# Kernel optimization log

Hardware: AMD Instinct MI355X
Metric: run time of the kernel (lower is better)

Reference implementation:

```python
import jax, jax.numpy as jnp
import numpy as np

N, E, IN_FEATS, D, H, DIST_DIM, NBOUND = 10000, 160000, 128, 64, 4, 32, 31

def setup_inputs() -> dict:
    key = jax.random.key(0)
    ks = jax.random.split(key, 16)
    gain = 5.0 / 3.0  # tanh gain
    def xavier(k, shape):
        # xavier_normal over the last two dims (fan_in, fan_out) as torch does per-slice
        fan_in, fan_out = shape[-2], shape[-1]
        std = gain * np.sqrt(2.0 / (fan_in + fan_out))
        return jax.random.normal(k, shape, dtype=jnp.float32) * std
    inp = {
        'feat': jax.random.normal(ks[0], (N, IN_FEATS), dtype=jnp.float32),
        'locations': jax.random.normal(ks[1], (N, 3), dtype=jnp.float32),
        'src': jax.random.randint(ks[2], (E,), 0, N),
        'dst': jax.random.randint(ks[3], (E,), 0, N),
        'inter_ids': jax.random.randint(ks[4], (E, H), 0, N),
        'W_fc': xavier(ks[5], (IN_FEATS, H * D)),
        'embed_table': jax.random.normal(ks[6], (NBOUND + 1, DIST_DIM), dtype=jnp.float32),
        'G': xavier(ks[7], (H, DIST_DIM, D)),
        'attn_fc1': xavier(ks[8], (H, 2 * D, D)),
        'attn_fc2': xavier(ks[9], (H, 2 * D, D)),
        'attn_fc3': xavier(ks[10], (H, 2 * D, D)),
        'attn_fc': xavier(ks[11], (H, 3 * D, D)),
        'attn_out': xavier(ks[12], (H, D, 1)),
        'boundaries': jnp.linspace(0.1, 3.1, NBOUND).astype(jnp.float32),
    }
    return inp


def reference(feat, locations, W_fc, embed_table, G, attn_fc1, attn_fc2, attn_fc3,
              attn_fc, attn_out, boundaries, src, dst, inter_ids):
    n = feat.shape[0]
    h = (feat @ W_fc).reshape(n, H, D)                      # [N,H,D]
    pos = locations                                          # [N,3]
    src_pos = pos[src]                                       # [E,3]
    dst_pos = pos[dst]                                       # [E,3]
    inter_pos = pos[inter_ids]                               # [E,H,3]
    h_src = h[src]                                           # [E,H,D]
    h_dst = h[dst]                                           # [E,H,D]
    head_idx = jnp.arange(H)[None, :]
    inter_h = h[inter_ids, head_idx, :]                      # [E,H,D] per-head gather

    e_count = src.shape[0]
    dist1 = jnp.broadcast_to(jnp.linalg.norm(dst_pos - src_pos, axis=-1)[:, None], (e_count, H))
    dist2 = jnp.linalg.norm(dst_pos[:, None, :] - inter_pos, axis=-1)   # [E,H]
    dist_ = jnp.linalg.norm(src_pos[:, None, :] - inter_pos, axis=-1)   # [E,H]

    def dist_embed(dist):
        idx = jnp.searchsorted(boundaries, dist, side='left')  # torch.bucketize(right=False)
        e = embed_table[idx]                                   # [E,H,DIST_DIM]
        return jnp.einsum('ehk,hkd->ehd', e, G)                # [E,H,D]

    de1 = dist_embed(dist1)
    de2 = dist_embed(dist2)
    de_ = dist_embed(dist_)

    d1 = jnp.einsum('ehk,hkd->ehd', jnp.concatenate([h_src, de1], axis=-1), attn_fc1)
    d2 = jnp.einsum('ehk,hkd->ehd', jnp.concatenate([inter_h, de2], axis=-1), attn_fc2)
    d3 = jnp.einsum('ehk,hkd->ehd', jnp.concatenate([h_dst, de_], axis=-1), attn_fc3)

    h_c = jnp.tanh(jnp.einsum('ehk,hkd->ehd', jnp.concatenate([d1, d2, d3], axis=-1), attn_fc))
    e_score = jnp.einsum('ehd,hdo->eho', h_c, attn_out)[..., 0]        # [E,H]

    # edge softmax grouped by destination node
    m = jax.ops.segment_max(e_score, dst, num_segments=n)              # [N,H]
    ex = jnp.exp(e_score - m[dst])
    den = jax.ops.segment_sum(ex, dst, num_segments=n)                 # [N,H]
    a = ex / den[dst]                                                  # [E,H]

    ft = jax.ops.segment_sum(a[:, :, None] * h_src, dst, num_segments=n)  # [N,H,D]
    rst = jnp.mean(ft, axis=1)                                          # merge='mean' -> [N,D]
    return rst
```

## Files before the change

### kernel.cpp

```cpp
#include <hip/hip_runtime.h>
#include <hip/hip_fp16.h>
#include <math.h>

#define N_NODES 10000
#define E_EDGES 160000
#define DMODEL 64
#define H 4
#define NBOUND 31
#define SLOTS 64
#define QREC 1024

typedef _Float16 half8 __attribute__((ext_vector_type(8)));
typedef float floatx4 __attribute__((ext_vector_type(4)));

__device__ __forceinline__ void mm4(const float* __restrict__ S, int aoff,
                                    int astride, int boff, int i0, int j,
                                    int Kdim, float o[4]) {
  float a0 = 0.f, a1 = 0.f, a2 = 0.f, a3 = 0.f;
  for (int t4 = 0; t4 < (Kdim >> 2); ++t4) {
    float4 f0 = *(const float4*)&S[aoff + (i0 + 0) * astride + t4 * 4];
    float4 f1 = *(const float4*)&S[aoff + (i0 + 1) * astride + t4 * 4];
    float4 f2 = *(const float4*)&S[aoff + (i0 + 2) * astride + t4 * 4];
    float4 f3 = *(const float4*)&S[aoff + (i0 + 3) * astride + t4 * 4];
    float b0 = S[boff + (t4 * 4 + 0) * 64 + j];
    float b1 = S[boff + (t4 * 4 + 1) * 64 + j];
    float b2 = S[boff + (t4 * 4 + 2) * 64 + j];
    float b3 = S[boff + (t4 * 4 + 3) * 64 + j];
    a0 += f0.x * b0 + f0.y * b1 + f0.z * b2 + f0.w * b3;
    a1 += f1.x * b0 + f1.y * b1 + f1.z * b2 + f1.w * b3;
    a2 += f2.x * b0 + f2.y * b1 + f2.z * b2 + f2.w * b3;
    a3 += f3.x * b0 + f3.y * b1 + f3.z * b2 + f3.w * b3;
  }
  o[0] = a0; o[1] = a1; o[2] = a2; o[3] = a3;
}

__device__ __forceinline__ int didx(const float* __restrict__ bnd2, float d) {
  int g = (int)(d * 10.0f);
  g = (g < 0) ? 0 : ((g > 31) ? 31 : g);
  g += (bnd2[g + 1] < d) ? 1 : 0;
  g -= (bnd2[g] >= d) ? 1 : 0;
  return g;
}

__global__ __launch_bounds__(512) void prep_kernel(
    const float* __restrict__ fc1, const float* __restrict__ fc2,
    const float* __restrict__ fc3, const float* __restrict__ fcc,
    const float* __restrict__ Wfc, const float* __restrict__ G,
    const float* __restrict__ emb, const float* __restrict__ pos,
    __half* __restrict__ bigWT, __half* __restrict__ U16,
    int* __restrict__ cnt, float4* __restrict__ pos4) {
  __shared__ __align__(16) float S[12288];
  int bi = blockIdx.x;
  int tid = threadIdx.x;
  if (bi >= 36) {
    int n = (bi - 36) * 512 + tid;
    if (n < N_NODES) {
      cnt[n] = 0;
      pos4[n] = make_float4(pos[n * 3], pos[n * 3 + 1], pos[n * 3 + 2], 0.f);
    }
    return;
  }
  int ca = bi / 12;
  int kh = bi % 12;
  int k = kh >> 2, h = kh & 3;
  const float* fck = (k == 0) ? fc1 : (k == 1) ? fc2 : fc3;
  fck += h * 128 * 64;
  const float* F = fcc + h * 192 * 64 + k * 64 * 64;
  int j = tid & 63, ig = tid >> 6;
  float o[4];
  if (ca < 2) {
    #pragma unroll
    for (int u = 0; u < 2; ++u) {
      ((float4*)S)[u * 512 + tid] = ((const float4*)F)[u * 512 + tid];
      ((float4*)(S + 4096))[u * 512 + tid] = ((const float4*)fck)[u * 512 + tid];
    }
    __syncthreads();
    #pragma unroll
    for (int rg = 0; rg < 2; ++rg) {
      int i0 = ig * 8 + rg * 4;
      mm4(S, 4096, 64, 0, i0, j, 64, o);
      S[8192 + (i0 + 0) * 64 + j] = o[0];
      S[8192 + (i0 + 1) * 64 + j] = o[1];
      S[8192 + (i0 + 2) * 64 + j] = o[2];
      S[8192 + (i0 + 3) * 64 + j] = o[3];
    }
    __syncthreads();
    int rbase = (ca == 0) ? 0 : 64;
    #pragma unroll
    for (int u = 0; u < 2; ++u) {
      int fi = u * 512 + tid;
      int i = fi >> 4, c4 = fi & 15;
      ((float4*)(S + 4096))[fi] =
          ((const float4*)(Wfc + (rbase + i) * 256 + h * 64))[c4];
    }
    __syncthreads();
    if (k == 0) {
      #pragma unroll
      for (int u = 0; u < 8; ++u) {
        int idx = u * 512 + tid;
        int i = idx >> 6, jj = idx & 63;
        bigWT[(h * 64 + jj) * 128 + rbase + i] = __float2half(S[4096 + idx]);
      }
    }
    #pragma unroll
    for (int rg = 0; rg < 2; ++rg) {
      int i0 = ig * 8 + rg * 4;
      mm4(S, 4096, 64, 8192, i0, j, 64, o);
      int rb = ((k + 1) * 256 + h * 64 + j) * 128 + rbase;
      bigWT[rb + i0 + 0] = __float2half(o[0]);
      bigWT[rb + i0 + 1] = __float2half(o[1]);
      bigWT[rb + i0 + 2] = __float2half(o[2]);
      bigWT[rb + i0 + 3] = __float2half(o[3]);
    }
    return;
  }
  #pragma unroll
  for (int u = 0; u < 2; ++u) {
    ((float4*)S)[u * 512 + tid] = ((const float4*)F)[u * 512 + tid];
    ((float4*)(S + 4096))[u * 512 + tid] =
        ((const float4*)(fck + 4096))[u * 512 + tid];
  }
  __syncthreads();
  #pragma unroll
  for (int rg = 0; rg < 2; ++rg) {
    int i0 = ig * 8 + rg * 4;
    mm4(S, 4096, 64, 0, i0, j, 64, o);
    S[8192 + (i0 + 0) * 64 + j] = o[0];
    S[8192 + (i0 + 1) * 64 + j] = o[1];
    S[8192 + (i0 + 2) * 64 + j] = o[2];
    S[8192 + (i0 + 3) * 64 + j] = o[3];
  }
  __syncthreads();
  ((float4*)S)[tid] = ((const float4*)(G + h * 2048))[tid];
  if (tid < 256) ((float4*)(S + 2048))[tid] = ((const float4*)emb)[tid];
  __syncthreads();
  {
    int i0 = ig * 4;
    mm4(S, 0, 64, 8192, i0, j, 64, o);
    S[3072 + (i0 + 0) * 64 + j] = o[0];
    S[3072 + (i0 + 1) * 64 + j] = o[1];
    S[3072 + (i0 + 2) * 64 + j] = o[2];
    S[3072 + (i0 + 3) * 64 + j] = o[3];
  }
  __syncthreads();
  {
    int i0 = ig * 4;
    mm4(S, 2048, 32, 3072, i0, j, 32, o);
    int base = k * 8192 + h * 2048;
    U16[base + (i0 + 0) * 64 + j] = __float2half(o[0]);
    U16[base + (i0 + 1) * 64 + j] = __float2half(o[1]);
    U16[base + (i0 + 2) * 64 + j] = __float2half(o[2]);
    U16[base + (i0 + 3) * 64 + j] = __float2half(o[3]);
  }
}

__global__ __launch_bounds__(256) void edge_kernel(
    const float4* __restrict__ pos4, const int* __restrict__ src,
    const int* __restrict__ dst, const int* __restrict__ inter,
    const float* __restrict__ boundaries, int* __restrict__ cnt,
    uint4* __restrict__ ebuf) {
  __shared__ float Sb[48];
  int tid = threadIdx.x;
  if (tid < NBOUND) Sb[tid + 1] = boundaries[tid];
  if (tid == NBOUND) { Sb[0] = -INFINITY; Sb[32] = INFINITY; }
  int e = blockIdx.x * 256 + tid;
  int s = src[e], t = dst[e];
  int p = atomicAdd(&cnt[t], 1);
  int4 iv = *(const int4*)&inter[e * 4];
  int itarr[4] = {iv.x, iv.y, iv.z, iv.w};
  float4 sp = pos4[s];
  float4 tp = pos4[t];
  float4 ip0 = pos4[itarr[0]];
  float4 ip1 = pos4[itarr[1]];
  float4 ip2 = pos4[itarr[2]];
  float4 ip3 = pos4[itarr[3]];
  __syncthreads();
  float dx = tp.x - sp.x, dy = tp.y - sp.y, dz = tp.z - sp.z;
  float dist1 = sqrtf(dx * dx + dy * dy + dz * dz);
  unsigned i1 = (unsigned)didx(Sb, dist1);
  float4 ips[4] = {ip0, ip1, ip2, ip3};
  unsigned w3 = 0, q20 = 0, q_0 = 0;
  #pragma unroll
  for (int hh = 0; hh < 4; ++hh) {
    float4 ip = ips[hh];
    float ax = tp.x - ip.x, ay = tp.y - ip.y, az = tp.z - ip.z;
    float dist2 = sqrtf(ax * ax + ay * ay + az * az);
    float bx = sp.x - ip.x, by = sp.y - ip.y, bz = sp.z - ip.z;
    float dist_ = sqrtf(bx * bx + by * by + bz * bz);
    unsigned idx2 = (unsigned)didx(Sb, dist2);
    unsigned idx_ = (unsigned)didx(Sb, dist_);
    if (hh == 0) { q20 = idx2; q_0 = idx_; }
    else w3 |= (idx2 | (idx_ << 5)) << ((hh - 1) * 10);
  }
  uint4 rec;
  rec.x = (unsigned)s | ((unsigned)itarr[0] << 16);
  rec.y = (unsigned)itarr[1] | ((unsigned)itarr[2] << 16);
  rec.z = (unsigned)itarr[3] | (i1 << 16) | (q20 << 21) | (q_0 << 26);
  rec.w = w3;
  if (p < SLOTS) ebuf[t * SLOTS + p] = rec;
}

#define EROW 264

__global__ __launch_bounds__(256) void gemm_kernel(
    const float* __restrict__ feat, const __half* __restrict__ bigWT,
    __half* __restrict__ qall) {
  __shared__ __align__(16) __half Esm[4][16][EROW];
  int bi = blockIdx.x;
  int tid = threadIdx.x;
  int bx = bi % 157, by = bi / 157;
  int wv = tid >> 6, l = tid & 63;
  int m0 = bx * 64 + wv * 16;
  int n0 = by * 256;
  int lm = l & 15, lk = (l >> 4) * 8;
  int arow = m0 + lm;
  if (arow >= N_NODES) arow = N_NODES - 1;
  const float* fp = feat + arow * 128 + lk;
  const _Float16* bp = (const _Float16*)bigWT + lk;
  half8 a[4];
  #pragma unroll
  for (int kt = 0; kt < 4; ++kt) {
    float4 u0 = *(const float4*)(fp + kt * 32);
    float4 u1 = *(const float4*)(fp + kt * 32 + 4);
    half8 t;
    t[0] = (_Float16)u0.x; t[1] = (_Float16)u0.y;
    t[2] = (_Float16)u0.z; t[3] = (_Float16)u0.w;
    t[4] = (_Float16)u1.x; t[5] = (_Float16)u1.y;
    t[6] = (_Float16)u1.z; t[7] = (_Float16)u1.w;
    a[kt] = t;
  }
  #pragma unroll
  for (int nt = 0; nt < 16; ++nt) {
    floatx4 acc = (floatx4){0.f, 0.f, 0.f, 0.f};
    #pragma unroll
    for (int kt = 0; kt < 4; ++kt) {
      half8 b = *(const half8*)(bp + (n0 + nt * 16 + lm) * 128 + kt * 32);
      acc = __builtin_amdgcn_mfma_f32_16x16x32_f16(a[kt], b, acc, 0, 0, 0);
    }
    int dd = nt * 16 + lm;
    #pragma unroll
    for (int r4 = 0; r4 < 4; ++r4)
      Esm[wv][(l >> 4) * 4 + r4][dd] = __float2half(acc[r4]);
  }
  __syncthreads();
  int row = l >> 2;
  int j0 = (l & 3) * 64;
  int m = m0 + row;
  if (m < N_NODES) {
    #pragma unroll
    for (int u = 0; u < 8; ++u) {
      uint4 v = *(const uint4*)&Esm[wv][row][j0 + u * 8];
      *(uint4*)&qall[m * QREC + by * 256 + j0 + u * 8] = v;
    }
  }
}

__device__ __forceinline__ float dpp_bfly_sum16(float v) {
  int x;
  x = __builtin_amdgcn_update_dpp(0, __float_as_int(v), 0xB1, 0xf, 0xf, true);
  v += __int_as_float(x);
  x = __builtin_amdgcn_update_dpp(0, __float_as_int(v), 0x4E, 0xf, 0xf, true);
  v += __int_as_float(x);
  x = __builtin_amdgcn_update_dpp(0, __float_as_int(v), 0x141, 0xf, 0xf, true);
  v += __int_as_float(x);
  x = __builtin_amdgcn_update_dpp(0, __float_as_int(v), 0x140, 0xf, 0xf, true);
  v += __int_as_float(x);
  return v;
}

union H4u { uint2 u; __half2 h[2]; };

__device__ __forceinline__ float tanh_dot(H4u A, H4u B, H4u C, H4u X, H4u Y,
                                          H4u Z, float4 a4) {
  __half2 z0 = __hadd2(__hadd2(A.h[0], B.h[0]), __hadd2(C.h[0], X.h[0]));
  z0 = __hadd2(z0, __hadd2(Y.h[0], Z.h[0]));
  __half2 z1 = __hadd2(__hadd2(A.h[1], B.h[1]), __hadd2(C.h[1], X.h[1]));
  z1 = __hadd2(z1, __hadd2(Y.h[1], Z.h[1]));
  float2 f0 = __half22float2(z0);
  float2 f1 = __half22float2(z1);
  const float K = 2.885390082f;
  float p0 = __builtin_amdgcn_exp2f(f0.x * K);
  float p1 = __builtin_amdgcn_exp2f(f0.y * K);
  float p2 = __builtin_amdgcn_exp2f(f1.x * K);
  float p3 = __builtin_amdgcn_exp2f(f1.y * K);
  float r0 = __builtin_amdgcn_rcpf(p0 + 1.0f);
  float r1 = __builtin_amdgcn_rcpf(p1 + 1.0f);
  float r2 = __builtin_amdgcn_rcpf(p2 + 1.0f);
  float r3 = __builtin_amdgcn_rcpf(p3 + 1.0f);
  float dot = a4.x * r0;
  dot = fmaf(a4.y, r1, dot);
  dot = fmaf(a4.z, r2, dot);
  dot = fmaf(a4.w, r3, dot);
  float asum = (a4.x + a4.y) + (a4.z + a4.w);
  return fmaf(-2.0f, dot, asum);
}

__device__ __forceinline__ float4 h4_to_f4(uint2 u) {
  union { uint2 ui; __half2 h[2]; } cc;
  cc.ui = u;
  float2 a = __half22float2(cc.h[0]);
  float2 b = __half22float2(cc.h[1]);
  return make_float4(a.x, a.y, b.x, b.y);
}

__device__ __forceinline__ void dec_rec(uint4 r, int h, int* s, int* it,
                                        unsigned* i1, unsigned* q2,
                                        unsigned* q_) {
  *s = (int)(r.x & 0xffff);
  *it = (h == 0) ? (int)(r.x >> 16)
      : (h == 1) ? (int)(r.y & 0xffff)
      : (h == 2) ? (int)(r.y >> 16) : (int)(r.z & 0xffff);
  *i1 = (r.z >> 16) & 31;
  if (h == 0) {
    *q2 = (r.z >> 21) & 31;
    *q_ = (r.z >> 26) & 31;
  } else {
    unsigned f = r.w >> ((h - 1) * 10);
    *q2 = f & 31;
    *q_ = (f >> 5) & 31;
  }
}

__global__ __launch_bounds__(256) void score_agg_kernel(
    const int* __restrict__ cnt, const uint4* __restrict__ ebuf,
    const __half* __restrict__ qall, const __half* __restrict__ U16,
    const float* __restrict__ aout, float* __restrict__ out) {
  __shared__ uint4 recs[SLOTS];
  __shared__ float4 sm_num[4][64];
  __shared__ float sm_den[4][4];
  int tid = threadIdx.x;
  int w = tid >> 6, lane = tid & 63;
  int h = lane >> 4, c = lane & 15;
  int n = blockIdx.x;
  int deg = cnt[n];
  if (deg > SLOTS) deg = SLOTS;
  if (tid < deg) recs[tid] = ebuf[n * SLOTS + tid];
  H4u C;
  C.u = *(const uint2*)(qall + n * QREC + 768 + h * 64 + c * 4);
  const float4 a4 = *((const float4*)(aout + h * 64) + c);
  __syncthreads();
  float4 num = make_float4(0.f, 0.f, 0.f, 0.f);
  float den = 0.f;
  int hc4 = h * 64 + c * 4;
  for (int i = w; i < deg; i += 8) {
    int iB = i + 4;
    int vB = (iB < deg);
    uint4 rA = recs[i];
    uint4 rB = recs[vB ? iB : i];
    int sA, itA, sB, itB;
    unsigned i1A, q2A, q_A, i1B, q2B, q_B;
    dec_rec(rA, h, &sA, &itA, &i1A, &q2A, &q_A);
    dec_rec(rB, h, &sB, &itB, &i1B, &q2B, &q_B);
    H4u A0, B0, X0, Y0, Z0, A1, B1, X1, Y1, Z1;
    uint2 hr0, hr1;
    hr0 = *(const uint2*)(qall + sA * QREC + hc4);
    A0.u = *(const uint2*)(qall + sA * QREC + 256 + hc4);
    B0.u = *(const uint2*)(qall + itA * QREC + 512 + hc4);
    X0.u = *(const uint2*)(U16 + (h * 32 + (int)i1A) * 64 + c * 4);
    Y0.u = *(const uint2*)(U16 + 8192 + (h * 32 + (int)q2A) * 64 + c * 4);
    Z0.u = *(const uint2*)(U16 + 16384 + (h * 32 + (int)q_A) * 64 + c * 4);
    hr1 = *(const uint2*)(qall + sB * QREC + hc4);
    A1.u = *(const uint2*)(qall + sB * QREC + 256 + hc4);
    B1.u = *(const uint2*)(qall + itB * QREC + 512 + hc4);
    X1.u = *(const uint2*)(U16 + (h * 32 + (int)i1B) * 64 + c * 4);
    Y1.u = *(const uint2*)(U16 + 8192 + (h * 32 + (int)q2B) * 64 + c * 4);
    Z1.u = *(const uint2*)(U16 + 16384 + (h * 32 + (int)q_B) * 64 + c * 4);
    float v0 = tanh_dot(A0, B0, C, X0, Y0, Z0, a4);
    float v1 = tanh_dot(A1, B1, C, X1, Y1, Z1, a4);
    v0 = dpp_bfly_sum16(v0);
    v1 = dpp_bfly_sum16(v1);
    float ex0 = __expf(v0);
    float ex1 = vB ? __expf(v1) : 0.f;
    float4 hv0 = h4_to_f4(hr0);
    float4 hv1 = h4_to_f4(hr1);
    num.x += ex0 * hv0.x + ex1 * hv1.x;
    num.y += ex0 * hv0.y + ex1 * hv1.y;
    num.z += ex0 * hv0.z + ex1 * hv1.z;
    num.w += ex0 * hv0.w + ex1 * hv1.w;
    den += ex0 + ex1;
  }
  sm_num[w][lane] = num;
  if (c == 0) sm_den[w][h] = den;
  __syncthreads();
  if (tid < 64) {
    float4 n0 = sm_num[0][lane], n1 = sm_num[1][lane];
    float4 n2 = sm_num[2][lane], n3 = sm_num[3][lane];
    float dt = sm_den[0][h] + sm_den[1][h] + sm_den[2][h] + sm_den[3][h];
    float4 t = make_float4(0.f, 0.f, 0.f, 0.f);
    if (deg > 0) {
      float inv = 1.0f / dt;
      t.x = (n0.x + n1.x + n2.x + n3.x) * inv;
      t.y = (n0.y + n1.y + n2.y + n3.y) * inv;
      t.z = (n0.z + n1.z + n2.z + n3.z) * inv;
      t.w = (n0.w + n1.w + n2.w + n3.w) * inv;
    }
    t.x += __shfl_xor(t.x, 16); t.y += __shfl_xor(t.y, 16);
    t.z += __shfl_xor(t.z, 16); t.w += __shfl_xor(t.w, 16);
    t.x += __shfl_xor(t.x, 32); t.y += __shfl_xor(t.y, 32);
    t.z += __shfl_xor(t.z, 32); t.w += __shfl_xor(t.w, 32);
    if (h == 0) {
      t.x *= 0.25f; t.y *= 0.25f; t.z *= 0.25f; t.w *= 0.25f;
      *(float4*)&out[n * 64 + c * 4] = t;
    }
  }
}

extern "C" void kernel_launch(void* const* d_in, const int* in_sizes, int n_in,
                              void* d_out, int out_size, void* d_ws,
                              size_t ws_size, hipStream_t stream) {
  const float* feat = (const float*)d_in[0];
  const float* loc = (const float*)d_in[1];
  const int* src = (const int*)d_in[2];
  const int* dst = (const int*)d_in[3];
  const int* inter = (const int*)d_in[4];
  const float* Wfc = (const float*)d_in[5];
  const float* emb = (const float*)d_in[6];
  const float* G = (const float*)d_in[7];
  const float* fc1 = (const float*)d_in[8];
  const float* fc2 = (const float*)d_in[9];
  const float* fc3 = (const float*)d_in[10];
  const float* fcc = (const float*)d_in[11];
  const float* aout = (const float*)d_in[12];
  const float* bnd = (const float*)d_in[13];
  float* out = (float*)d_out;

  __half* qall = (__half*)d_ws;
  __half* bigWT = qall + N_NODES * QREC;
  __half* U16 = bigWT + 1024 * 128;
  uint4* ebuf = (uint4*)(U16 + 3 * H * 2048);
  int* cnt = (int*)(ebuf + N_NODES * SLOTS);
  float4* pos4 = (float4*)(cnt + N_NODES);

  prep_kernel<<<56, 512, 0, stream>>>(fc1, fc2, fc3, fcc, Wfc, G, emb, loc,
                                      bigWT, U16, cnt, pos4);
  edge_kernel<<<E_EDGES / 256, 256, 0, stream>>>(pos4, src, dst, inter, bnd,
                                                 cnt, ebuf);
  gemm_kernel<<<628, 256, 0, stream>>>(feat, bigWT, qall);
  score_agg_kernel<<<N_NODES, 256, 0, stream>>>(cnt, ebuf, qall, U16, aout,
                                                out);
}
```

Before: 182.2 us.

## Fuse edge preprocessing, U16 precompute and node GEMM into one launch

The edge binning kernel, the distance-embedding table precompute and the node GEMM now run as block ranges of a single fused kernel launch. The prep kernel keeps only the bigWT weight folding and the node init. This removes one kernel launch and the serialization between the edge and GEMM stages, letting their blocks overlap. The cost is a shared-memory union sized for the GEMM path and heterogeneous blocks whose durations differ.

```diff
diff --git a/kernel.cpp b/kernel.cpp
--- a/kernel.cpp
+++ b/kernel.cpp
@@ -45,15 +45,14 @@
 __global__ __launch_bounds__(512) void prep_kernel(
     const float* __restrict__ fc1, const float* __restrict__ fc2,
     const float* __restrict__ fc3, const float* __restrict__ fcc,
-    const float* __restrict__ Wfc, const float* __restrict__ G,
-    const float* __restrict__ emb, const float* __restrict__ pos,
-    __half* __restrict__ bigWT, __half* __restrict__ U16,
-    int* __restrict__ cnt, float4* __restrict__ pos4) {
+    const float* __restrict__ Wfc, const float* __restrict__ pos,
+    __half* __restrict__ bigWT, int* __restrict__ cnt,
+    float4* __restrict__ pos4) {
   __shared__ __align__(16) float S[12288];
   int bi = blockIdx.x;
   int tid = threadIdx.x;
-  if (bi >= 36) {
-    int n = (bi - 36) * 512 + tid;
+  if (bi >= 24) {
+    int n = (bi - 24) * 512 + tid;
     if (n < N_NODES) {
       cnt[n] = 0;
       pos4[n] = make_float4(pos[n * 3], pos[n * 3 + 1], pos[n * 3 + 2], 0.f);
@@ -68,57 +67,10 @@
   const float* F = fcc + h * 192 * 64 + k * 64 * 64;
   int j = tid & 63, ig = tid >> 6;
   float o[4];
-  if (ca < 2) {
-    #pragma unroll
-    for (int u = 0; u < 2; ++u) {
-      ((float4*)S)[u * 512 + tid] = ((const float4*)F)[u * 512 + tid];
-      ((float4*)(S + 4096))[u * 512 + tid] = ((const float4*)fck)[u * 512 + tid];
-    }
-    __syncthreads();
-    #pragma unroll
-    for (int rg = 0; rg < 2; ++rg) {
-      int i0 = ig * 8 + rg * 4;
-      mm4(S, 4096, 64, 0, i0, j, 64, o);
-      S[8192 + (i0 + 0) * 64 + j] = o[0];
-      S[8192 + (i0 + 1) * 64 + j] = o[1];
-      S[8192 + (i0 + 2) * 64 + j] = o[2];
-      S[8192 + (i0 + 3) * 64 + j] = o[3];
-    }
-    __syncthreads();
-    int rbase = (ca == 0) ? 0 : 64;
-    #pragma unroll
-    for (int u = 0; u < 2; ++u) {
-      int fi = u * 512 + tid;
-      int i = fi >> 4, c4 = fi & 15;
-      ((float4*)(S + 4096))[fi] =
-          ((const float4*)(Wfc + (rbase + i) * 256 + h * 64))[c4];
-    }
-    __syncthreads();
-    if (k == 0) {
-      #pragma unroll
-      for (int u = 0; u < 8; ++u) {
-        int idx = u * 512 + tid;
-        int i = idx >> 6, jj = idx & 63;
-        bigWT[(h * 64 + jj) * 128 + rbase + i] = __float2half(S[4096 + idx]);
-      }
-    }
-    #pragma unroll
-    for (int rg = 0; rg < 2; ++rg) {
-      int i0 = ig * 8 + rg * 4;
-      mm4(S, 4096, 64, 8192, i0, j, 64, o);
-      int rb = ((k + 1) * 256 + h * 64 + j) * 128 + rbase;
-      bigWT[rb + i0 + 0] = __float2half(o[0]);
-      bigWT[rb + i0 + 1] = __float2half(o[1]);
-      bigWT[rb + i0 + 2] = __float2half(o[2]);
-      bigWT[rb + i0 + 3] = __float2half(o[3]);
-    }
-    return;
-  }
   #pragma unroll
   for (int u = 0; u < 2; ++u) {
     ((float4*)S)[u * 512 + tid] = ((const float4*)F)[u * 512 + tid];
-    ((float4*)(S + 4096))[u * 512 + tid] =
-        ((const float4*)(fck + 4096))[u * 512 + tid];
+    ((float4*)(S + 4096))[u * 512 + tid] = ((const float4*)fck)[u * 512 + tid];
   }
   __syncthreads();
   #pragma unroll
@@ -131,84 +83,156 @@
     S[8192 + (i0 + 3) * 64 + j] = o[3];
   }
   __syncthreads();
-  ((float4*)S)[tid] = ((const float4*)(G + h * 2048))[tid];
-  if (tid < 256) ((float4*)(S + 2048))[tid] = ((const float4*)emb)[tid];
-  __syncthreads();
-  {
-    int i0 = ig * 4;
-    mm4(S, 0, 64, 8192, i0, j, 64, o);
-    S[3072 + (i0 + 0) * 64 + j] = o[0];
-    S[3072 + (i0 + 1) * 64 + j] = o[1];
-    S[3072 + (i0 + 2) * 64 + j] = o[2];
-    S[3072 + (i0 + 3) * 64 + j] = o[3];
-  }
-  __syncthreads();
-  {
-    int i0 = ig * 4;
-    mm4(S, 2048, 32, 3072, i0, j, 32, o);
-    int base = k * 8192 + h * 2048;
-    U16[base + (i0 + 0) * 64 + j] = __float2half(o[0]);
-    U16[base + (i0 + 1) * 64 + j] = __float2half(o[1]);
-    U16[base + (i0 + 2) * 64 + j] = __float2half(o[2]);
-    U16[base + (i0 + 3) * 64 + j] = __float2half(o[3]);
-  }
-}
-
-__global__ __launch_bounds__(256) void edge_kernel(
-    const float4* __restrict__ pos4, const int* __restrict__ src,
-    const int* __restrict__ dst, const int* __restrict__ inter,
-    const float* __restrict__ boundaries, int* __restrict__ cnt,
-    uint4* __restrict__ ebuf) {
-  __shared__ float Sb[48];
-  int tid = threadIdx.x;
-  if (tid < NBOUND) Sb[tid + 1] = boundaries[tid];
-  if (tid == NBOUND) { Sb[0] = -INFINITY; Sb[32] = INFINITY; }
-  int e = blockIdx.x * 256 + tid;
-  int s = src[e], t = dst[e];
-  int p = atomicAdd(&cnt[t], 1);
-  int4 iv = *(const int4*)&inter[e * 4];
-  int itarr[4] = {iv.x, iv.y, iv.z, iv.w};
-  float4 sp = pos4[s];
-  float4 tp = pos4[t];
-  float4 ip0 = pos4[itarr[0]];
-  float4 ip1 = pos4[itarr[1]];
-  float4 ip2 = pos4[itarr[2]];
-  float4 ip3 = pos4[itarr[3]];
-  __syncthreads();
-  float dx = tp.x - sp.x, dy = tp.y - sp.y, dz = tp.z - sp.z;
-  float dist1 = sqrtf(dx * dx + dy * dy + dz * dz);
-  unsigned i1 = (unsigned)didx(Sb, dist1);
-  float4 ips[4] = {ip0, ip1, ip2, ip3};
-  unsigned w3 = 0, q20 = 0, q_0 = 0;
-  #pragma unroll
-  for (int hh = 0; hh < 4; ++hh) {
-    float4 ip = ips[hh];
-    float ax = tp.x - ip.x, ay = tp.y - ip.y, az = tp.z - ip.z;
-    float dist2 = sqrtf(ax * ax + ay * ay + az * az);
-    float bx = sp.x - ip.x, by = sp.y - ip.y, bz = sp.z - ip.z;
-    float dist_ = sqrtf(bx * bx + by * by + bz * bz);
-    unsigned idx2 = (unsigned)didx(Sb, dist2);
-    unsigned idx_ = (unsigned)didx(Sb, dist_);
-    if (hh == 0) { q20 = idx2; q_0 = idx_; }
-    else w3 |= (idx2 | (idx_ << 5)) << ((hh - 1) * 10);
-  }
-  uint4 rec;
-  rec.x = (unsigned)s | ((unsigned)itarr[0] << 16);
-  rec.y = (unsigned)itarr[1] | ((unsigned)itarr[2] << 16);
-  rec.z = (unsigned)itarr[3] | (i1 << 16) | (q20 << 21) | (q_0 << 26);
-  rec.w = w3;
-  if (p < SLOTS) ebuf[t * SLOTS + p] = rec;
+  int rbase = (ca == 0) ? 0 : 64;
+  #pragma unroll
+  for (int u = 0; u < 2; ++u) {
+    int fi = u * 512 + tid;
+    int i = fi >> 4, c4 = fi & 15;
+    ((float4*)(S + 4096))[fi] =
+        ((const float4*)(Wfc + (rbase + i) * 256 + h * 64))[c4];
+  }
+  __syncthreads();
+  if (k == 0) {
+    #pragma unroll
+    for (int u = 0; u < 8; ++u) {
+      int idx = u * 512 + tid;
+      int i = idx >> 6, jj = idx & 63;
+      bigWT[(h * 64 + jj) * 128 + rbase + i] = __float2half(S[4096 + idx]);
+    }
+  }
+  #pragma unroll
+  for (int rg = 0; rg < 2; ++rg) {
+    int i0 = ig * 8 + rg * 4;
+    mm4(S, 4096, 64, 8192, i0, j, 64, o);
+    int rb = ((k + 1) * 256 + h * 64 + j) * 128 + rbase;
+    bigWT[rb + i0 + 0] = __float2half(o[0]);
+    bigWT[rb + i0 + 1] = __float2half(o[1]);
+    bigWT[rb + i0 + 2] = __float2half(o[2]);
+    bigWT[rb + i0 + 3] = __float2half(o[3]);
+  }
 }
 
 #define EROW 264
-
-__global__ __launch_bounds__(256) void gemm_kernel(
+#define SMEM_BYTES 33792
+
+__global__ __launch_bounds__(256) void fused_kernel(
     const float* __restrict__ feat, const __half* __restrict__ bigWT,
-    __half* __restrict__ qall) {
-  __shared__ __align__(16) __half Esm[4][16][EROW];
+    __half* __restrict__ qall, const float4* __restrict__ pos4,
+    const int* __restrict__ src, const int* __restrict__ dst,
+    const int* __restrict__ inter, const float* __restrict__ boundaries,
+    int* __restrict__ cnt, uint4* __restrict__ ebuf,
+    const float* __restrict__ fc1, const float* __restrict__ fc2,
+    const float* __restrict__ fc3, const float* __restrict__ fcc,
+    const float* __restrict__ G, const float* __restrict__ emb,
+    __half* __restrict__ U16) {
+  __shared__ __align__(16) char smem[SMEM_BYTES];
   int bi = blockIdx.x;
   int tid = threadIdx.x;
-  int bx = bi % 157, by = bi / 157;
+  if (bi < 12) {
+    float* S = (float*)smem;
+    int k = bi >> 2, h = bi & 3;
+    const float* fck = (k == 0) ? fc1 : (k == 1) ? fc2 : fc3;
+    fck += h * 128 * 64;
+    const float* F = fcc + h * 192 * 64 + k * 64 * 64;
+    int j = tid & 63, ig = tid >> 6;
+    #pragma unroll
+    for (int u = 0; u < 4; ++u) {
+      ((float4*)S)[u * 256 + tid] = ((const float4*)F)[u * 256 + tid];
+      ((float4*)(S + 4096))[u * 256 + tid] =
+          ((const float4*)(fck + 4096))[u * 256 + tid];
+    }
+    __syncthreads();
+    float ob[4][4];
+    #pragma unroll
+    for (int rg = 0; rg < 4; ++rg)
+      mm4(S, 4096, 64, 0, ig * 16 + rg * 4, j, 64, ob[rg]);
+    __syncthreads();
+    #pragma unroll
+    for (int rg = 0; rg < 4; ++rg) {
+      int i0 = ig * 16 + rg * 4;
+      S[(i0 + 0) * 64 + j] = ob[rg][0];
+      S[(i0 + 1) * 64 + j] = ob[rg][1];
+      S[(i0 + 2) * 64 + j] = ob[rg][2];
+      S[(i0 + 3) * 64 + j] = ob[rg][3];
+    }
+    #pragma unroll
+    for (int u = 0; u < 2; ++u)
+      ((float4*)(S + 4096))[u * 256 + tid] =
+          ((const float4*)(G + h * 2048))[u * 256 + tid];
+    ((float4*)(S + 6144))[tid] = ((const float4*)emb)[tid];
+    __syncthreads();
+    float og[2][4];
+    #pragma unroll
+    for (int rg = 0; rg < 2; ++rg)
+      mm4(S, 4096, 64, 0, ig * 8 + rg * 4, j, 64, og[rg]);
+    __syncthreads();
+    #pragma unroll
+    for (int rg = 0; rg < 2; ++rg) {
+      int i0 = ig * 8 + rg * 4;
+      S[(i0 + 0) * 64 + j] = og[rg][0];
+      S[(i0 + 1) * 64 + j] = og[rg][1];
+      S[(i0 + 2) * 64 + j] = og[rg][2];
+      S[(i0 + 3) * 64 + j] = og[rg][3];
+    }
+    __syncthreads();
+    float o[4];
+    #pragma unroll
+    for (int rg = 0; rg < 2; ++rg) {
+      int i0 = ig * 8 + rg * 4;
+      mm4(S, 6144, 32, 0, i0, j, 32, o);
+      int base = k * 8192 + h * 2048;
+      U16[base + (i0 + 0) * 64 + j] = __float2half(o[0]);
+      U16[base + (i0 + 1) * 64 + j] = __float2half(o[1]);
+      U16[base + (i0 + 2) * 64 + j] = __float2half(o[2]);
+      U16[base + (i0 + 3) * 64 + j] = __float2half(o[3]);
+    }
+    return;
+  }
+  if (bi >= 640) {
+    float* Sb = (float*)smem;
+    if (tid < NBOUND) Sb[tid + 1] = boundaries[tid];
+    if (tid == NBOUND) { Sb[0] = -INFINITY; Sb[32] = INFINITY; }
+    int e = (bi - 640) * 256 + tid;
+    int s = src[e], t = dst[e];
+    int p = atomicAdd(&cnt[t], 1);
+    int4 iv = *(const int4*)&inter[e * 4];
+    int itarr[4] = {iv.x, iv.y, iv.z, iv.w};
+    float4 sp = pos4[s];
+    float4 tp = pos4[t];
+    float4 ip0 = pos4[itarr[0]];
+    float4 ip1 = pos4[itarr[1]];
+    float4 ip2 = pos4[itarr[2]];
+    float4 ip3 = pos4[itarr[3]];
+    __syncthreads();
+    float dx = tp.x - sp.x, dy = tp.y - sp.y, dz = tp.z - sp.z;
+    float dist1 = sqrtf(dx * dx + dy * dy + dz * dz);
+    unsigned i1 = (unsigned)didx(Sb, dist1);
+    float4 ips[4] = {ip0, ip1, ip2, ip3};
+    unsigned w3 = 0, q20 = 0, q_0 = 0;
+    #pragma unroll
+    for (int hh = 0; hh < 4; ++hh) {
+      float4 ip = ips[hh];
+      float ax = tp.x - ip.x, ay = tp.y - ip.y, az = tp.z - ip.z;
+      float dist2 = sqrtf(ax * ax + ay * ay + az * az);
+      float bx = sp.x - ip.x, by = sp.y - ip.y, bz = sp.z - ip.z;
+      float dist_ = sqrtf(bx * bx + by * by + bz * bz);
+      unsigned idx2 = (unsigned)didx(Sb, dist2);
+      unsigned idx_ = (unsigned)didx(Sb, dist_);
+      if (hh == 0) { q20 = idx2; q_0 = idx_; }
+      else w3 |= (idx2 | (idx_ << 5)) << ((hh - 1) * 10);
+    }
+    uint4 rec;
+    rec.x = (unsigned)s | ((unsigned)itarr[0] << 16);
+    rec.y = (unsigned)itarr[1] | ((unsigned)itarr[2] << 16);
+    rec.z = (unsigned)itarr[3] | (i1 << 16) | (q20 << 21) | (q_0 << 26);
+    rec.w = w3;
+    if (p < SLOTS) ebuf[t * SLOTS + p] = rec;
+    return;
+  }
+  typedef __half EsmT[16][EROW];
+  EsmT* Esm = (EsmT*)smem;
+  int gi = bi - 12;
+  int bx = gi % 157, by = gi / 157;
   int wv = tid >> 6, l = tid & 63;
   int m0 = bx * 64 + wv * 16;
   int n0 = by * 256;
@@ -431,11 +455,11 @@
   int* cnt = (int*)(ebuf + N_NODES * SLOTS);
   float4* pos4 = (float4*)(cnt + N_NODES);
 
-  prep_kernel<<<56, 512, 0, stream>>>(fc1, fc2, fc3, fcc, Wfc, G, emb, loc,
-                                      bigWT, U16, cnt, pos4);
-  edge_kernel<<<E_EDGES / 256, 256, 0, stream>>>(pos4, src, dst, inter, bnd,
-                                                 cnt, ebuf);
-  gemm_kernel<<<628, 256, 0, stream>>>(feat, bigWT, qall);
+  prep_kernel<<<44, 512, 0, stream>>>(fc1, fc2, fc3, fcc, Wfc, loc, bigWT,
+                                      cnt, pos4);
+  fused_kernel<<<1265, 256, 0, stream>>>(feat, bigWT, qall, pos4, src, dst,
+                                         inter, bnd, cnt, ebuf, fc1, fc2, fc3,
+                                         fcc, G, emb, U16);
   score_agg_kernel<<<N_NODES, 256, 0, stream>>>(cnt, ebuf, qall, U16, aout,
                                                 out);
 }
```

Measured after the change: 173.8 us. 4.6% less time.
